# Optimization experiments

Hardware: AMD Instinct MI355X
Metric: run time of the kernel (lower is better)

The kernel has to match this reference:

```python
import jax, jax.numpy as jnp
import numpy as np

NUM_HEADS = 8
DIM_KEY = 64
WINDOW = 16
TEMP = float(np.power(DIM_KEY, 0.5))


def setup_inputs() -> dict:
    key = jax.random.key(0)
    k1, k2, k3, k4 = jax.random.split(key, 4)
    B, T, H = 4, 2048, 512
    std = np.sqrt(2.0 / (H + DIM_KEY))
    return {
        "query": jax.random.normal(k1, (B, T, H), dtype=jnp.float32),
        "key": jax.random.normal(k2, (B, T, H), dtype=jnp.float32),
        "Wq": jax.random.normal(k3, (NUM_HEADS * DIM_KEY, H), dtype=jnp.float32) * std,
        "bq": jnp.zeros((NUM_HEADS * DIM_KEY,), dtype=jnp.float32),
        "Wk": jax.random.normal(k4, (NUM_HEADS * DIM_KEY, H), dtype=jnp.float32) * std,
        "bk": jnp.zeros((NUM_HEADS * DIM_KEY,), dtype=jnp.float32),
    }


def reference(query, key, Wq, bq, Wk, bk):
    B, T, _ = query.shape
    w = WINDOW
    # linear projections, split into heads: [B, T, H, dk]
    q = (jnp.einsum("bti,oi->bto", query, Wq) + bq).reshape(B, T, NUM_HEADS, DIM_KEY)
    k = (jnp.einsum("bti,oi->bto", key, Wk) + bk).reshape(B, T, NUM_HEADS, DIM_KEY)
    # dense scores [B, H, Tq, Tk]
    attn = jnp.einsum("bqhd,bkhd->bhqk", q, k) / TEMP
    # window mask (get_window_mask): allowed where i-w <= j <= i+w
    i = jnp.arange(T)[:, None]
    j = jnp.arange(T)[None, :]
    allowed = (j >= i - w) & (j <= i + w)  # [T, T]
    attn = jnp.where(allowed[None, None], attn, -jnp.inf)
    attn = jax.nn.softmax(attn, axis=-1)
    # select mask gather (get_select_mask): each row keeps 2w+1 cols
    # starting at clip(i - w, 0, T - (2w+1))
    starts = jnp.clip(jnp.arange(T) - w, 0, T - (2 * w + 1))  # [T]
    idx = starts[:, None] + jnp.arange(2 * w + 1)[None, :]  # [T, 2w+1]
    out = jnp.take_along_axis(attn, idx[None, None, :, :], axis=-1)
    return out  # [B, NUM_HEADS, T, 2w+1]
```

## Files before the change

kernel.cpp:

```cpp
#include <hip/hip_runtime.h>
#include <hip/hip_bf16.h>
#include <math.h>

#define TT 2048
#define HH 512
#define NH 8
#define DK 64
#define WIN 16
#define NC 33
#define MT 8192

typedef __attribute__((ext_vector_type(8))) short bf16x8;
typedef __attribute__((ext_vector_type(4))) float f32x4;

__device__ inline ushort f2bf(float f) {
  uint u = __builtin_bit_cast(uint, f);
  return (ushort)((u + 0x7FFFu + ((u >> 16) & 1u)) >> 16);
}
__device__ inline ushort cvt1(float f) {
  __hip_bfloat16 h = __float2bfloat16(f);
  return __builtin_bit_cast(ushort, h);
}

__global__ __launch_bounds__(512, 2) void fused_mha(
    const float* __restrict__ qin, const float* __restrict__ kin,
    const float* __restrict__ Wq, const float* __restrict__ Wk,
    const float* __restrict__ bq, const float* __restrict__ bk,
    float* __restrict__ out)
{
  __shared__ ushort lds[26624];

  const int m0 = blockIdx.x * 64;
  const int n0 = blockIdx.y * 128;
  const int t  = threadIdx.x;
  const int w  = t >> 6;
  const int l  = t & 63;
  const int lr = l & 15;
  const int hi = l >> 4;
  const int swz = lr & 7;

  const bool isQA  = (w < 4);
  const int  rowA  = (isQA ? w : w - 4) * 16;
  const int  ldsAA = isQA ? 0 : 4096;
  const int  ldsWA = isQA ? 10240 : 18432;
  const bool hasB  = (w < 2);
  const int  rowB  = (4 + w) * 16;

  f32x4 accA[8] = {};
  f32x4 accB[8] = {};

  for (int k0 = 0; k0 < HH; k0 += 64) {
#pragma unroll
    for (int p = 0; p < 7; ++p) {
      const int u = p * 512 + t;
      if (p < 6 || t < 256) {
        const float* src; int base, lg;
        if (u < 512)       { lg = u;        const int r = lg >> 3; src = qin + (size_t)(m0 + r) * HH; base = 0; }
        else if (u < 1280) { lg = u - 512;  int r = lg >> 3; int ar = m0 - 16 + r;
                             ar = ar < 0 ? 0 : (ar > MT - 1 ? MT - 1 : ar);
                             src = kin + (size_t)ar * HH; base = 4096; }
        else if (u < 2304) { lg = u - 1280; const int r = lg >> 3; src = Wq + (size_t)(n0 + r) * HH; base = 10240; }
        else               { lg = u - 2304; const int r = lg >> 3; src = Wk + (size_t)(n0 + r) * HH; base = 18432; }
        const int rr = lg >> 3;
        const int g  = (lg & 7) ^ (rr & 7);
        const float* gp = src + k0 + g * 8;
        float4 x = ((const float4*)gp)[0], y = ((const float4*)gp)[1];
        union { ushort s[8]; uint4 v; } pk;
        pk.s[0]=cvt1(x.x); pk.s[1]=cvt1(x.y); pk.s[2]=cvt1(x.z); pk.s[3]=cvt1(x.w);
        pk.s[4]=cvt1(y.x); pk.s[5]=cvt1(y.y); pk.s[6]=cvt1(y.z); pk.s[7]=cvt1(y.w);
        *(uint4*)&lds[base + lg * 8] = pk.v;
      }
    }
    __syncthreads();

#pragma unroll
    for (int kk = 0; kk < 64; kk += 32) {
      const int gq = (kk >> 3) + hi;
      bf16x8 afA = *(const bf16x8*)&lds[ldsAA + (rowA + lr) * 64 + ((gq ^ swz) * 8)];
#pragma unroll
      for (int n = 0; n < 8; ++n) {
        bf16x8 bw = *(const bf16x8*)&lds[ldsWA + (n * 16 + lr) * 64 + ((gq ^ swz) * 8)];
        accA[n] = __builtin_amdgcn_mfma_f32_16x16x32_bf16(afA, bw, accA[n], 0, 0, 0);
      }
      if (hasB) {
        bf16x8 afB = *(const bf16x8*)&lds[4096 + (rowB + lr) * 64 + ((gq ^ swz) * 8)];
#pragma unroll
        for (int n = 0; n < 8; ++n) {
          bf16x8 bw = *(const bf16x8*)&lds[18432 + (n * 16 + lr) * 64 + ((gq ^ swz) * 8)];
          accB[n] = __builtin_amdgcn_mfma_f32_16x16x32_bf16(afB, bw, accB[n], 0, 0, 0);
        }
      }
    }
    __syncthreads();
  }

  {
    const float* biasA = isQA ? bq : bk;
    const int pbaseA = isQA ? 0 : 8192;
#pragma unroll
    for (int n = 0; n < 8; ++n) {
      const float bc = biasA[n0 + n * 16 + lr];
      const int c = n * 16 + lr;
#pragma unroll
      for (int q_ = 0; q_ < 4; ++q_) {
        const int row = rowA + hi * 4 + q_;
        lds[pbaseA + row * 128 + (((c >> 3) ^ (row & 7)) << 3) + (c & 7)] =
            f2bf(accA[n][q_] + bc);
      }
    }
    if (hasB) {
#pragma unroll
      for (int n = 0; n < 8; ++n) {
        const float bc = bk[n0 + n * 16 + lr];
        const int c = n * 16 + lr;
#pragma unroll
        for (int q_ = 0; q_ < 4; ++q_) {
          const int row = rowB + hi * 4 + q_;
          lds[8192 + row * 128 + (((c >> 3) ^ (row & 7)) << 3) + (c & 7)] =
              f2bf(accB[n][q_] + bc);
        }
      }
    }
  }
  __syncthreads();

  const int s  = w & 3;
  const int hl = w >> 2;
  const int bb = m0 >> 11;
  const int ml = m0 & (TT - 1);
  const int i0l = ml + s * 16;

  int jbt = i0l - WIN;
  if (jbt < 0) jbt = 0;
  if (jbt > TT - NC) jbt = TT - NC;
  const int krb = jbt - ml + 16;

  f32x4 acc[3] = {};
#pragma unroll
  for (int kk = 0; kk < 64; kk += 32) {
    const int gc = hl * 8 + (kk >> 3) + hi;
    const int rowq = s * 16 + lr;
    bf16x8 aq = *(const bf16x8*)&lds[rowq * 128 + (((gc) ^ (rowq & 7)) << 3)];
#pragma unroll
    for (int a = 0; a < 3; ++a) {
      const int kr = krb + a * 16 + lr;
      bf16x8 bkf = *(const bf16x8*)&lds[8192 + kr * 128 + (((gc) ^ (kr & 7)) << 3)];
      acc[a] = __builtin_amdgcn_mfma_f32_16x16x32_bf16(aq, bkf, acc[a], 0, 0, 0);
    }
  }

  float e[3][4];
  float inv[4];
#pragma unroll
  for (int q_ = 0; q_ < 4; ++q_) {
    const int i = i0l + hi * 4 + q_;
    const int j0 = jbt + lr, j1 = j0 + 16, j2 = j0 + 32;
    float s0 = (j0 >= i - WIN && j0 <= i + WIN && j0 < TT) ? acc[0][q_] * 0.125f : -INFINITY;
    float s1 = (j1 >= i - WIN && j1 <= i + WIN && j1 < TT) ? acc[1][q_] * 0.125f : -INFINITY;
    float s2 = (j2 >= i - WIN && j2 <= i + WIN && j2 < TT) ? acc[2][q_] * 0.125f : -INFINITY;
    float m = fmaxf(fmaxf(s0, s1), s2);
#pragma unroll
    for (int off = 8; off; off >>= 1) m = fmaxf(m, __shfl_xor(m, off));
    const float e0 = __expf(s0 - m);
    const float e1 = __expf(s1 - m);
    const float e2 = __expf(s2 - m);
    e[0][q_] = e0; e[1][q_] = e1; e[2][q_] = e2;
    float sum = e0 + e1 + e2;
#pragma unroll
    for (int off = 8; off; off >>= 1) sum += __shfl_xor(sum, off);
    inv[q_] = 1.0f / sum;
  }

  const int h = blockIdx.y * 2 + hl;
  const size_t obase = ((size_t)(bb * NH + h)) * TT * NC;
#pragma unroll
  for (int q_ = 0; q_ < 4; ++q_) {
    const int i = i0l + hi * 4 + q_;
    int st = i - WIN;
    if (st < 0) st = 0;
    if (st > TT - NC) st = TT - NC;
#pragma unroll
    for (int a = 0; a < 3; ++a) {
      const int c = jbt + a * 16 + lr - st;
      if (c >= 0 && c < NC)
        out[obase + (size_t)i * NC + c] = e[a][q_] * inv[q_];
    }
  }
}

extern "C" void kernel_launch(void* const* d_in, const int* in_sizes, int n_in,
                              void* d_out, int out_size, void* d_ws, size_t ws_size,
                              hipStream_t stream)
{
  const float* query = (const float*)d_in[0];
  const float* key   = (const float*)d_in[1];
  const float* Wq    = (const float*)d_in[2];
  const float* bq    = (const float*)d_in[3];
  const float* Wk    = (const float*)d_in[4];
  const float* bk    = (const float*)d_in[5];
  float* out = (float*)d_out;

  fused_mha<<<dim3(MT / 64, 4), 512, 0, stream>>>(
      query, key, Wq, Wk, bq, bk, out);
}
```

Before: 37.89 us.

## Pre-convert weights to bf16 and load via direct global-to-LDS copies

A separate kernel converts Wq and Wk to bf16 once per call into workspace. The fused kernel then streams these bf16 weights straight into LDS with global_load_lds, which halves weight read bytes and skips the per-tile conversion that every block repeated. The projection GEMM work is also rebalanced so all 8 waves do equal work (5 row tiles × 2 column tiles each) instead of 4+2 uneven waves, and the occupancy hint rises to 4 blocks per CU. The trade-off is an extra kernel launch plus a workspace round trip, and the raised occupancy hint may add register pressure.

```diff
diff --git a/kernel.cpp b/kernel.cpp
--- a/kernel.cpp
+++ b/kernel.cpp
@@ -22,9 +22,25 @@
   return __builtin_bit_cast(ushort, h);
 }
 
-__global__ __launch_bounds__(512, 2) void fused_mha(
+__global__ __launch_bounds__(256) void cvt_w(
+    const float* __restrict__ Wq, const float* __restrict__ Wk,
+    ushort* __restrict__ Wqb, ushort* __restrict__ Wkb)
+{
+  const int id = blockIdx.x * 256 + threadIdx.x;
+  const float* src = (id < 32768) ? Wq : Wk;
+  ushort* dst = (id < 32768) ? Wqb : Wkb;
+  const int off = (id & 32767) * 8;
+  float4 x = *(const float4*)(src + off);
+  float4 y = *(const float4*)(src + off + 4);
+  union { ushort s[8]; uint4 v; } pk;
+  pk.s[0]=cvt1(x.x); pk.s[1]=cvt1(x.y); pk.s[2]=cvt1(x.z); pk.s[3]=cvt1(x.w);
+  pk.s[4]=cvt1(y.x); pk.s[5]=cvt1(y.y); pk.s[6]=cvt1(y.z); pk.s[7]=cvt1(y.w);
+  *(uint4*)(dst + off) = pk.v;
+}
+
+__global__ __launch_bounds__(512, 4) void fused_mha(
     const float* __restrict__ qin, const float* __restrict__ kin,
-    const float* __restrict__ Wq, const float* __restrict__ Wk,
+    const ushort* __restrict__ Wqb, const ushort* __restrict__ Wkb,
     const float* __restrict__ bq, const float* __restrict__ bk,
     float* __restrict__ out)
 {
@@ -38,29 +54,34 @@
   const int lr = l & 15;
   const int hi = l >> 4;
   const int swz = lr & 7;
-
-  const bool isQA  = (w < 4);
-  const int  rowA  = (isQA ? w : w - 4) * 16;
-  const int  ldsAA = isQA ? 0 : 4096;
-  const int  ldsWA = isQA ? 10240 : 18432;
-  const bool hasB  = (w < 2);
-  const int  rowB  = (4 + w) * 16;
-
-  f32x4 accA[8] = {};
-  f32x4 accB[8] = {};
+  const int wr2 = w >> 2;
+  const int wc2 = w & 3;
+
+  f32x4 acc[5][2] = {};
 
   for (int k0 = 0; k0 < HH; k0 += 64) {
 #pragma unroll
-    for (int p = 0; p < 7; ++p) {
+    for (int p = 0; p < 4; ++p) {
+      const int u2 = p * 512 + t;
+      const int lg = (u2 < 1024) ? u2 : u2 - 1024;
+      const int r  = lg >> 3;
+      const int g  = (lg & 7) ^ (r & 7);
+      const ushort* src = ((u2 < 1024) ? Wqb : Wkb) + (size_t)(n0 + r) * HH + k0 + g * 8;
+      const int base = (u2 < 1024) ? 10240 : 18432;
+      __builtin_amdgcn_global_load_lds(
+          (const __attribute__((address_space(1))) uint*)src,
+          (__attribute__((address_space(3))) uint*)(lds + base + lg * 8),
+          16, 0, 0);
+    }
+#pragma unroll
+    for (int p = 0; p < 3; ++p) {
       const int u = p * 512 + t;
-      if (p < 6 || t < 256) {
+      if (p < 2 || t < 256) {
         const float* src; int base, lg;
-        if (u < 512)       { lg = u;        const int r = lg >> 3; src = qin + (size_t)(m0 + r) * HH; base = 0; }
-        else if (u < 1280) { lg = u - 512;  int r = lg >> 3; int ar = m0 - 16 + r;
-                             ar = ar < 0 ? 0 : (ar > MT - 1 ? MT - 1 : ar);
-                             src = kin + (size_t)ar * HH; base = 4096; }
-        else if (u < 2304) { lg = u - 1280; const int r = lg >> 3; src = Wq + (size_t)(n0 + r) * HH; base = 10240; }
-        else               { lg = u - 2304; const int r = lg >> 3; src = Wk + (size_t)(n0 + r) * HH; base = 18432; }
+        if (u < 512) { lg = u; const int r = lg >> 3; src = qin + (size_t)(m0 + r) * HH; base = 0; }
+        else         { lg = u - 512; const int r = lg >> 3; int ar = m0 - 16 + r;
+                       ar = ar < 0 ? 0 : (ar > MT - 1 ? MT - 1 : ar);
+                       src = kin + (size_t)ar * HH; base = 4096; }
         const int rr = lg >> 3;
         const int g  = (lg & 7) ^ (rr & 7);
         const float* gp = src + k0 + g * 8;
@@ -76,49 +97,44 @@
 #pragma unroll
     for (int kk = 0; kk < 64; kk += 32) {
       const int gq = (kk >> 3) + hi;
-      bf16x8 afA = *(const bf16x8*)&lds[ldsAA + (rowA + lr) * 64 + ((gq ^ swz) * 8)];
-#pragma unroll
-      for (int n = 0; n < 8; ++n) {
-        bf16x8 bw = *(const bf16x8*)&lds[ldsWA + (n * 16 + lr) * 64 + ((gq ^ swz) * 8)];
-        accA[n] = __builtin_amdgcn_mfma_f32_16x16x32_bf16(afA, bw, accA[n], 0, 0, 0);
-      }
-      if (hasB) {
-        bf16x8 afB = *(const bf16x8*)&lds[4096 + (rowB + lr) * 64 + ((gq ^ swz) * 8)];
-#pragma unroll
-        for (int n = 0; n < 8; ++n) {
-          bf16x8 bw = *(const bf16x8*)&lds[18432 + (n * 16 + lr) * 64 + ((gq ^ swz) * 8)];
-          accB[n] = __builtin_amdgcn_mfma_f32_16x16x32_bf16(afB, bw, accB[n], 0, 0, 0);
-        }
+      bf16x8 bqf[2], bkf[2];
+#pragma unroll
+      for (int cc = 0; cc < 2; ++cc) {
+        const int crow = (wc2 * 2 + cc) * 16 + lr;
+        bqf[cc] = *(const bf16x8*)&lds[10240 + crow * 64 + ((gq ^ swz) * 8)];
+        bkf[cc] = *(const bf16x8*)&lds[18432 + crow * 64 + ((gq ^ swz) * 8)];
+      }
+#pragma unroll
+      for (int j = 0; j < 5; ++j) {
+        const int srow = wr2 * 5 + j;
+        const bool isq = (srow < 4);
+        const int abase = isq ? 0 : 4096;
+        const int arow  = (isq ? srow : srow - 4) * 16 + lr;
+        bf16x8 af = *(const bf16x8*)&lds[abase + arow * 64 + ((gq ^ swz) * 8)];
+#pragma unroll
+        for (int cc = 0; cc < 2; ++cc)
+          acc[j][cc] = __builtin_amdgcn_mfma_f32_16x16x32_bf16(
+              af, isq ? bqf[cc] : bkf[cc], acc[j][cc], 0, 0, 0);
       }
     }
     __syncthreads();
   }
 
-  {
-    const float* biasA = isQA ? bq : bk;
-    const int pbaseA = isQA ? 0 : 8192;
-#pragma unroll
-    for (int n = 0; n < 8; ++n) {
-      const float bc = biasA[n0 + n * 16 + lr];
-      const int c = n * 16 + lr;
+#pragma unroll
+  for (int j = 0; j < 5; ++j) {
+    const int srow = wr2 * 5 + j;
+    const bool isq = (srow < 4);
+    const int pbase = isq ? 0 : 8192;
+    const int rowt  = (isq ? srow : srow - 4) * 16;
+#pragma unroll
+    for (int cc = 0; cc < 2; ++cc) {
+      const int c2 = (wc2 * 2 + cc) * 16 + lr;
+      const float bc = (isq ? bq : bk)[n0 + c2];
 #pragma unroll
       for (int q_ = 0; q_ < 4; ++q_) {
-        const int row = rowA + hi * 4 + q_;
-        lds[pbaseA + row * 128 + (((c >> 3) ^ (row & 7)) << 3) + (c & 7)] =
-            f2bf(accA[n][q_] + bc);
-      }
-    }
-    if (hasB) {
-#pragma unroll
-      for (int n = 0; n < 8; ++n) {
-        const float bc = bk[n0 + n * 16 + lr];
-        const int c = n * 16 + lr;
-#pragma unroll
-        for (int q_ = 0; q_ < 4; ++q_) {
-          const int row = rowB + hi * 4 + q_;
-          lds[8192 + row * 128 + (((c >> 3) ^ (row & 7)) << 3) + (c & 7)] =
-              f2bf(accB[n][q_] + bc);
-        }
+        const int row = rowt + hi * 4 + q_;
+        lds[pbase + row * 128 + (((c2 >> 3) ^ (row & 7)) << 3) + (c2 & 7)] =
+            f2bf(acc[j][cc][q_] + bc);
       }
     }
   }
@@ -135,17 +151,17 @@
   if (jbt > TT - NC) jbt = TT - NC;
   const int krb = jbt - ml + 16;
 
-  f32x4 acc[3] = {};
+  f32x4 acc3[3] = {};
 #pragma unroll
   for (int kk = 0; kk < 64; kk += 32) {
     const int gc = hl * 8 + (kk >> 3) + hi;
     const int rowq = s * 16 + lr;
-    bf16x8 aq = *(const bf16x8*)&lds[rowq * 128 + (((gc) ^ (rowq & 7)) << 3)];
+    bf16x8 aq = *(const bf16x8*)&lds[rowq * 128 + ((gc ^ (rowq & 7)) << 3)];
 #pragma unroll
     for (int a = 0; a < 3; ++a) {
       const int kr = krb + a * 16 + lr;
-      bf16x8 bkf = *(const bf16x8*)&lds[8192 + kr * 128 + (((gc) ^ (kr & 7)) << 3)];
-      acc[a] = __builtin_amdgcn_mfma_f32_16x16x32_bf16(aq, bkf, acc[a], 0, 0, 0);
+      bf16x8 bkfr = *(const bf16x8*)&lds[8192 + kr * 128 + ((gc ^ (kr & 7)) << 3)];
+      acc3[a] = __builtin_amdgcn_mfma_f32_16x16x32_bf16(aq, bkfr, acc3[a], 0, 0, 0);
     }
   }
 
@@ -155,9 +171,9 @@
   for (int q_ = 0; q_ < 4; ++q_) {
     const int i = i0l + hi * 4 + q_;
     const int j0 = jbt + lr, j1 = j0 + 16, j2 = j0 + 32;
-    float s0 = (j0 >= i - WIN && j0 <= i + WIN && j0 < TT) ? acc[0][q_] * 0.125f : -INFINITY;
-    float s1 = (j1 >= i - WIN && j1 <= i + WIN && j1 < TT) ? acc[1][q_] * 0.125f : -INFINITY;
-    float s2 = (j2 >= i - WIN && j2 <= i + WIN && j2 < TT) ? acc[2][q_] * 0.125f : -INFINITY;
+    float s0 = (j0 >= i - WIN && j0 <= i + WIN && j0 < TT) ? acc3[0][q_] * 0.125f : -INFINITY;
+    float s1 = (j1 >= i - WIN && j1 <= i + WIN && j1 < TT) ? acc3[1][q_] * 0.125f : -INFINITY;
+    float s2 = (j2 >= i - WIN && j2 <= i + WIN && j2 < TT) ? acc3[2][q_] * 0.125f : -INFINITY;
     float m = fmaxf(fmaxf(s0, s1), s2);
 #pragma unroll
     for (int off = 8; off; off >>= 1) m = fmaxf(m, __shfl_xor(m, off));
@@ -200,6 +216,10 @@
   const float* bk    = (const float*)d_in[5];
   float* out = (float*)d_out;
 
+  ushort* Wqb = (ushort*)d_ws;
+  ushort* Wkb = Wqb + (size_t)HH * HH;
+
+  cvt_w<<<dim3(256), 256, 0, stream>>>(Wq, Wk, Wqb, Wkb);
   fused_mha<<<dim3(MT / 64, 4), 512, 0, stream>>>(
-      query, key, Wq, Wk, bq, bk, out);
-}
+      query, key, Wqb, Wkb, bq, bk, out);
+}
```

Result: faster. 33.29 us, median of 2 (-12.1%).
